# Performance work log

Hardware: AMD Instinct MI355X
Metric: run time of the kernel (lower is better)

Reference implementation:

```python
import jax, jax.numpy as jnp
import numpy as np

N_NODES = 100000
N_EDGES = 1280000
D_IN = 64
D_HID = 64


def _sage_conv(x, src, dst, deg, Wl, bl, Wr):
    # gather source-node features per edge, scatter-mean to destination nodes
    msg = x[src]                                            # [E, d]
    agg = jax.ops.segment_sum(msg, dst, num_segments=N_NODES)  # [N, d]
    mean = agg / deg                                        # [N, d]
    # PyG SAGEConv: lin_l(aggregated) + lin_r(root); bias lives in lin_l
    return mean @ Wl.T + bl + x @ Wr.T


def setup_inputs() -> dict:
    key = jax.random.key(0)
    ks = jax.random.split(key, 10)
    x = jax.random.normal(ks[0], (N_NODES, D_IN), dtype=jnp.float32)
    edge_index = jax.random.randint(ks[1], (2, N_EDGES), 0, N_NODES, dtype=jnp.int64)
    s = 1.0 / np.sqrt(D_IN)
    W1l = jax.random.uniform(ks[2], (D_HID, D_IN), jnp.float32, -s, s)
    W1r = jax.random.uniform(ks[3], (D_HID, D_IN), jnp.float32, -s, s)
    b1 = jax.random.uniform(ks[4], (D_HID,), jnp.float32, -s, s)
    s2 = 1.0 / np.sqrt(D_HID)
    W2l = jax.random.uniform(ks[5], (D_HID, D_HID), jnp.float32, -s2, s2)
    W2r = jax.random.uniform(ks[6], (D_HID, D_HID), jnp.float32, -s2, s2)
    b2 = jax.random.uniform(ks[7], (D_HID,), jnp.float32, -s2, s2)
    Wh = jax.random.uniform(ks[8], (1, D_HID), jnp.float32, -s2, s2)
    bh = jax.random.uniform(ks[9], (1,), jnp.float32, -s2, s2)
    return {"x": x, "edge_index": edge_index, "W1l": W1l, "W1r": W1r, "b1": b1,
            "W2l": W2l, "W2r": W2r, "b2": b2, "Wh": Wh, "bh": bh}


def reference(x, edge_index, W1l, W1r, b1, W2l, W2r, b2, Wh, bh):
    src, dst = edge_index[0], edge_index[1]
    # in-degree for mean aggregation (clamped to avoid div-by-zero)
    deg = jax.ops.segment_sum(jnp.ones((N_EDGES,), jnp.float32), dst,
                              num_segments=N_NODES)
    deg = jnp.maximum(deg, 1.0)[:, None]                    # [N, 1]
    h = jax.nn.relu(_sage_conv(x, src, dst, deg, W1l, b1, W1r))
    h = jax.nn.relu(_sage_conv(h, src, dst, deg, W2l, b2, W2r))
    out = (h @ Wh.T + bh)[:, 0]                             # [N]
    return out, h
```

## Files before the change

kernel.cpp:

```cpp
#include <hip/hip_runtime.h>

#define N_NODES 100000
#define N_EDGES 1280000
#define D 64
#define NPAD 102400
#define CAP 48
#define NBUCK 391
#define AB 313
#define CVB 1024
#define NT32 3125
#define XQ (N_NODES * 16)

typedef __attribute__((ext_vector_type(8))) short bf16x8;
typedef __attribute__((ext_vector_type(4))) float f32x4;
typedef __attribute__((ext_vector_type(2))) float f32x2;

__device__ __forceinline__ unsigned short f2bf(float f) {
    union { float f; unsigned u; } c; c.f = f;
    unsigned u = c.u;
    return (unsigned short)((u + 0x7FFF + ((u >> 16) & 1)) >> 16);
}
__device__ __forceinline__ float bf2f(unsigned short s) {
    union { unsigned u; float f; } c; c.u = ((unsigned)s) << 16;
    return c.f;
}
__device__ __forceinline__ float fp8d(unsigned b) {
    unsigned t = ((b & 0x80u) << 24) | ((b & 0x7fu) << 20);
    union { unsigned u; float f; } c; c.u = t;
    return c.f * 1.32922799578491587e36f;
}
__device__ __forceinline__ unsigned char f2fp8(float f) {
    f = fminf(fmaxf(f, -448.f), 448.f);
    float g = f * 7.52316384526264005e-37f;
    union { float f; unsigned u; } c; c.f = g;
    unsigned gb = c.u;
    unsigned r = (((gb & 0x7fffffffu) + 0x7ffffu + ((gb >> 20) & 1u)) >> 20) & 0x7fu;
    return (unsigned char)(((gb >> 24) & 0x80u) | r);
}

__global__ __launch_bounds__(512) void prep_kernel(
    const float* __restrict__ x,
    const int* __restrict__ src, const int* __restrict__ dst,
    const float* __restrict__ W1l, const float* __restrict__ W1r,
    const float* __restrict__ W2l, const float* __restrict__ W2r,
    unsigned short* __restrict__ xb, unsigned short* __restrict__ h1b,
    unsigned char* __restrict__ x8, unsigned char* __restrict__ h8,
    unsigned short* __restrict__ wb,
    int* __restrict__ sorted, int* __restrict__ exclT)
{
    __shared__ int cntA[392];
    __shared__ int excl[512];
    __shared__ int stage_pk[4096];

    const int t   = threadIdx.x;
    const int bid = blockIdx.x;

    if (bid < AB) {
        const int e0 = bid * 4096;
        const int cbatch = min(4096, N_EDGES - e0);

        if (t < 392) cntA[t] = 0;
        __syncthreads();

        int mb[8], mr[8], mpk[8];
#pragma unroll
        for (int i = 0; i < 8; ++i) {
            int idx = i * 512 + t;
            mb[i] = -1;
            if (idx < cbatch) {
                int e = e0 + idx;
                int s = src[e], d = dst[e];
                int b = d >> 8;
                mb[i]  = b;
                mpk[i] = (s << 8) | (d & 255);
                mr[i]  = atomicAdd(&cntA[b], 1);
            }
        }
        __syncthreads();

        excl[t] = (t < 392) ? cntA[t] : 0;
        __syncthreads();
        for (int off = 1; off < 512; off <<= 1) {
            int u = (t >= off) ? excl[t - off] : 0;
            __syncthreads();
            excl[t] += u;
            __syncthreads();
        }

#pragma unroll
        for (int i = 0; i < 8; ++i) {
            if (mb[i] >= 0) {
                int b = mb[i];
                stage_pk[excl[b] - cntA[b] + mr[i]] = mpk[i];
            }
        }
        __syncthreads();

#pragma unroll
        for (int i = 0; i < 8; ++i) {
            int idx = i * 512 + t;
            if (idx < cbatch) sorted[e0 + idx] = stage_pk[idx];
        }
        if (t < 392) exclT[bid * 392 + t] = excl[t] - cntA[t];
    } else {
        const int gtid = (bid - AB) * 512 + t;
        const int gsz  = CVB * 512;
        const int TOT  = XQ + 32 + 4096;
        for (int i = gtid; i < TOT; i += gsz) {
            if (i < XQ) {
                float4 v = ((const float4*)x)[i];
                ((ushort4*)xb)[i] = make_ushort4(f2bf(v.x), f2bf(v.y), f2bf(v.z), f2bf(v.w));
                ((uchar4*)x8)[i]  = make_uchar4(f2fp8(v.x), f2fp8(v.y), f2fp8(v.z), f2fp8(v.w));
            } else if (i < XQ + 32) {
                int k = i - XQ;
                if (k < 16) {
                    ((ushort4*)xb)[(size_t)N_NODES * 16 + k] = make_ushort4(0,0,0,0);
                    ((unsigned*)x8)[(size_t)N_NODES * 16 + k] = 0u;
                } else {
                    ((ushort4*)h1b)[(size_t)N_NODES * 16 + (k - 16)] = make_ushort4(0,0,0,0);
                    ((unsigned*)h8)[(size_t)N_NODES * 16 + (k - 16)] = 0u;
                }
            } else {
                int wf = i - XQ - 32;
                int m = wf >> 10, k = wf & 1023;
                const float* s = (m == 0) ? W1l : (m == 1) ? W1r : (m == 2) ? W2l : W2r;
                float4 v = ((const float4*)s)[k];
                ((ushort4*)wb)[m * 1024 + k] =
                    make_ushort4(f2bf(v.x), f2bf(v.y), f2bf(v.z), f2bf(v.w));
            }
        }
    }
}

__global__ __launch_bounds__(512) void binB_kernel(const int* __restrict__ sorted,
                                                   const int* __restrict__ exclT,
                                                   int* __restrict__ csr,
                                                   int* __restrict__ deg) {
    __shared__ int cur[256];
    __shared__ __align__(16) int lcsr[256 * CAP];
    __shared__ int scan[512];
    __shared__ int segstart[314];
    __shared__ int segsrc[313];

    const int t = threadIdx.x;
    const int k = blockIdx.x;

    if (t < 256) cur[t] = 0;

    int cnt = 0, s0 = 0;
    if (t < AB) {
        s0  = exclT[t * 392 + k];
        cnt = exclT[t * 392 + k + 1] - s0;
    }
    scan[t] = (t < AB) ? cnt : 0;
    __syncthreads();
    for (int off = 1; off < 512; off <<= 1) {
        int u = (t >= off) ? scan[t - off] : 0;
        __syncthreads();
        scan[t] += u;
        __syncthreads();
    }
    if (t < AB) {
        segstart[t] = scan[t] - cnt;
        segsrc[t]   = t * 4096 + s0;
    }
    if (t == AB - 1) segstart[AB] = scan[AB - 1];
    __syncthreads();

    const int Tk = segstart[AB];
    for (int i = t; i < Tk; i += 512) {
        int lo = 0, hi = AB;
        while (hi - lo > 1) {
            int mid = (lo + hi) >> 1;
            if (segstart[mid] <= i) lo = mid; else hi = mid;
        }
        int pk = sorted[segsrc[lo] + (i - segstart[lo])];
        int nl = pk & 255;
        int s  = pk >> 8;
        int r  = atomicAdd(&cur[nl], 1);
        if (r < CAP) lcsr[nl * CAP + r] = s;
    }
    __syncthreads();

    const int base = k * 256;
    for (int i = t; i < 4096; i += 512) {
        int r = i >> 4, c = i & 15;
        if (c < 12) {
            int lenr = min(cur[r], CAP);
            if (c * 4 < lenr)
                *(int4*)(csr + (size_t)(base + r) * CAP + c * 4) =
                    *(const int4*)(lcsr + r * CAP + c * 4);
        }
    }
    if (t < 256) deg[base + t] = cur[t];
}

template <int LAYER>
__global__ __launch_bounds__(512) void layer_kernel(
    const int* __restrict__ csr, const int* __restrict__ deg_g,
    const unsigned char*  __restrict__ feat8,
    const unsigned short* __restrict__ root_b,
    const unsigned short* __restrict__ wl_b,
    const float* __restrict__ bl,
    const unsigned short* __restrict__ wr_b,
    unsigned short* __restrict__ hout_b,
    unsigned char*  __restrict__ hout8,
    float* __restrict__ hout_f,
    const float* __restrict__ Wh, const float* __restrict__ bh,
    float* __restrict__ out)
{
    __shared__ __align__(16) char lds[10240];
    unsigned short* sA = (unsigned short*)lds;
    unsigned short* sX = sA + 32 * 72;
    float* sH    = (float*)lds;
    float* spart = (float*)(lds + 9216);

    const int tid = threadIdx.x;
    const int n0  = blockIdx.x * 32;

    {
        int row = tid >> 4, c4 = tid & 15;
        ushort4 x4 = ((const ushort4*)root_b)[(n0 + row) * 16 + c4];
        *(ushort4*)(sX + row * 72 + c4 * 4) = x4;
    }

    {
        const uint2* fb2 = (const uint2*)feat8;
        const int g   = tid >> 4;
        const int l   = tid & 15;
        const int h   = l >> 3;
        const int lo  = l & 7;
        const int n   = n0 + g;
        const int dg  = deg_g[n];
        const int len = (dg < CAP) ? dg : CAP;
        const int* rp = csr + n * CAP;
        f32x2 a0 = {0.f, 0.f}, a1 = {0.f, 0.f}, a2 = {0.f, 0.f}, a3 = {0.f, 0.f};
        for (int cb = 0; cb < len; cb += 16) {
            int idxl = cb + l;
            int id = (idxl < len) ? rp[idxl] : N_NODES;
            uint2 w[8];
#pragma unroll
            for (int i = 0; i < 8; ++i)
                w[i] = fb2[(__shfl(id, 2 * i + h, 16) << 3) + lo];
#pragma unroll
            for (int i = 0; i < 8; ++i) {
#if __has_builtin(__builtin_amdgcn_cvt_pk_f32_fp8)
                a0 += __builtin_amdgcn_cvt_pk_f32_fp8((int)w[i].x, false);
                a1 += __builtin_amdgcn_cvt_pk_f32_fp8((int)w[i].x, true);
                a2 += __builtin_amdgcn_cvt_pk_f32_fp8((int)w[i].y, false);
                a3 += __builtin_amdgcn_cvt_pk_f32_fp8((int)w[i].y, true);
#else
                f32x2 p0 = {fp8d(w[i].x & 255), fp8d((w[i].x >> 8) & 255)};
                f32x2 p1 = {fp8d((w[i].x >> 16) & 255), fp8d(w[i].x >> 24)};
                f32x2 p2 = {fp8d(w[i].y & 255), fp8d((w[i].y >> 8) & 255)};
                f32x2 p3 = {fp8d((w[i].y >> 16) & 255), fp8d(w[i].y >> 24)};
                a0 += p0; a1 += p1; a2 += p2; a3 += p3;
#endif
            }
        }
        a0.x += __shfl_xor(a0.x, 8); a0.y += __shfl_xor(a0.y, 8);
        a1.x += __shfl_xor(a1.x, 8); a1.y += __shfl_xor(a1.y, 8);
        a2.x += __shfl_xor(a2.x, 8); a2.y += __shfl_xor(a2.y, 8);
        a3.x += __shfl_xor(a3.x, 8); a3.y += __shfl_xor(a3.y, 8);
        float inv = 1.0f / fmaxf((float)dg, 1.0f);
        if (h == 0) {
            *(ushort4*)(sA + g * 72 + lo * 8) =
                make_ushort4(f2bf(a0.x * inv), f2bf(a0.y * inv),
                             f2bf(a1.x * inv), f2bf(a1.y * inv));
            *(ushort4*)(sA + g * 72 + lo * 8 + 4) =
                make_ushort4(f2bf(a2.x * inv), f2bf(a2.y * inv),
                             f2bf(a3.x * inv), f2bf(a3.y * inv));
        }
    }
    __syncthreads();

    const int w8 = tid >> 6;
    const int rt = w8 & 1, jt = w8 >> 1;
    const int l64 = tid & 63;
    const int rowl = l64 & 15, quad = l64 >> 4;

    const unsigned short* ap = sA + (rt * 16 + rowl) * 72 + quad * 8;
    const unsigned short* xp = sX + (rt * 16 + rowl) * 72 + quad * 8;
    bf16x8 am0 = *(const bf16x8*)(ap);
    bf16x8 am1 = *(const bf16x8*)(ap + 32);
    bf16x8 ax0 = *(const bf16x8*)(xp);
    bf16x8 ax1 = *(const bf16x8*)(xp + 32);
    __syncthreads();

    const unsigned short* wlp = wl_b + (jt * 16 + rowl) * 64 + quad * 8;
    const unsigned short* wrp = wr_b + (jt * 16 + rowl) * 64 + quad * 8;
    bf16x8 b0 = *(const bf16x8*)(wlp);
    bf16x8 b1 = *(const bf16x8*)(wlp + 32);
    bf16x8 b2 = *(const bf16x8*)(wrp);
    bf16x8 b3 = *(const bf16x8*)(wrp + 32);
    f32x4 acc = {0.f, 0.f, 0.f, 0.f};
    acc = __builtin_amdgcn_mfma_f32_16x16x32_bf16(am0, b0, acc, 0, 0, 0);
    acc = __builtin_amdgcn_mfma_f32_16x16x32_bf16(am1, b1, acc, 0, 0, 0);
    acc = __builtin_amdgcn_mfma_f32_16x16x32_bf16(ax0, b2, acc, 0, 0, 0);
    acc = __builtin_amdgcn_mfma_f32_16x16x32_bf16(ax1, b3, acc, 0, 0, 0);
    float bj = bl[jt * 16 + rowl];

#pragma unroll
    for (int r = 0; r < 4; ++r) {
        int node = rt * 16 + quad * 4 + r;
        sH[node * 68 + jt * 16 + rowl] = fmaxf(acc[r] + bj, 0.f);
    }
    __syncthreads();

    if (LAYER == 2 && tid < 256) {
        int node = tid >> 3, q = tid & 7;
        float p = 0.f;
#pragma unroll
        for (int c = 0; c < 2; ++c) {
            float4 hv = *(const float4*)(sH + node * 68 + q * 8 + c * 4);
            float4 wv = ((const float4*)Wh)[q * 2 + c];
            p += hv.x * wv.x + hv.y * wv.y + hv.z * wv.z + hv.w * wv.w;
        }
        spart[tid] = p;
    }

    {
        int row = tid >> 4, c4 = tid & 15;
        int n = n0 + row;
        const float* hp = sH + row * 68 + c4 * 4;
        if (LAYER == 1) {
            ((ushort4*)hout_b)[n * 16 + c4] =
                make_ushort4(f2bf(hp[0]), f2bf(hp[1]), f2bf(hp[2]), f2bf(hp[3]));
            ((uchar4*)hout8)[n * 16 + c4] =
                make_uchar4(f2fp8(hp[0]), f2fp8(hp[1]), f2fp8(hp[2]), f2fp8(hp[3]));
        } else {
            ((float4*)hout_f)[n * 16 + c4] =
                make_float4(hp[0], hp[1], hp[2], hp[3]);
        }
    }

    if (LAYER == 2) {
        __syncthreads();
        if (tid < 32) {
            float s = bh[0];
#pragma unroll
            for (int q = 0; q < 8; ++q) s += spart[tid * 8 + q];
            out[n0 + tid] = s;
        }
    }
}

extern "C" void kernel_launch(void* const* d_in, const int* in_sizes, int n_in,
                              void* d_out, int out_size, void* d_ws, size_t ws_size,
                              hipStream_t stream) {
    const float* x   = (const float*)d_in[0];
    const int*   ei  = (const int*)d_in[1];
    const int*   src = ei;
    const int*   dst = ei + N_EDGES;
    const float* W1l = (const float*)d_in[2];
    const float* W1r = (const float*)d_in[3];
    const float* b1  = (const float*)d_in[4];
    const float* W2l = (const float*)d_in[5];
    const float* W2r = (const float*)d_in[6];
    const float* b2  = (const float*)d_in[7];
    const float* Wh  = (const float*)d_in[8];
    const float* bh  = (const float*)d_in[9];

    float* out   = (float*)d_out;
    float* h_out = out + N_NODES;

    int* wsi = (int*)d_ws;
    int* deg = wsi;
    int* csr = deg + NPAD;
    unsigned short* wb  = (unsigned short*)(csr + NBUCK * 256 * CAP);
    unsigned short* x_b = wb + 16384;
    unsigned short* h1b = x_b + (size_t)(N_NODES + 1) * D;
    unsigned char*  x8  = (unsigned char*)(h1b + (size_t)(N_NODES + 1) * D);
    unsigned char*  h8  = x8 + (size_t)(N_NODES + 1) * D;
    int* sorted = (int*)h1b;
    int* exclT  = sorted + AB * 4096;

    unsigned short* w1l_b = wb;
    unsigned short* w1r_b = wb + 4096;
    unsigned short* w2l_b = wb + 8192;
    unsigned short* w2r_b = wb + 12288;

    prep_kernel<<<AB + CVB, 512, 0, stream>>>(
        x, src, dst, W1l, W1r, W2l, W2r, x_b, h1b, x8, h8, wb, sorted, exclT);

    binB_kernel<<<NBUCK, 512, 0, stream>>>(sorted, exclT, csr, deg);

    layer_kernel<1><<<NT32, 512, 0, stream>>>(
        csr, deg, x8, x_b, w1l_b, b1, w1r_b, h1b, h8, nullptr,
        nullptr, nullptr, nullptr);
    layer_kernel<2><<<NT32, 512, 0, stream>>>(
        csr, deg, h8, h1b, w2l_b, b2, w2r_b, nullptr, nullptr, h_out,
        Wh, bh, out);
}
```

Measured before the change: 181.7 us.

## Fuse all four kernels into one persistent kernel with grid barriers

Replaces the prep, binning and two layer launches with a single persistent kernel that loops over the same work items and separates phases with atomic-counter grid barriers. The grid is sized from the occupancy query and capped at 512 blocks, and a memset resets the barrier counter before each launch. The aim is to remove launch gaps and tail effects between the four kernels. In exchange it adds barrier spin overhead and a larger shared-memory footprint, which may lower occupancy during the layer phases. It also relies on every block being co-resident.

```diff
diff --git a/kernel.cpp b/kernel.cpp
--- a/kernel.cpp
+++ b/kernel.cpp
@@ -7,9 +7,13 @@
 #define CAP 48
 #define NBUCK 391
 #define AB 313
-#define CVB 1024
+#define NCVT 711
 #define NT32 3125
 #define XQ (N_NODES * 16)
+#define CVTOT (XQ + 32 + 4096)
+#define CVW ((CVTOT + NCVT - 1) / NCVT)
+#define GRID 512
+#define SMEM_BYTES 52688
 
 typedef __attribute__((ext_vector_type(8))) short bf16x8;
 typedef __attribute__((ext_vector_type(4))) float f32x4;
@@ -19,10 +23,6 @@
     union { float f; unsigned u; } c; c.f = f;
     unsigned u = c.u;
     return (unsigned short)((u + 0x7FFF + ((u >> 16) & 1)) >> 16);
-}
-__device__ __forceinline__ float bf2f(unsigned short s) {
-    union { unsigned u; float f; } c; c.u = ((unsigned)s) << 16;
-    return c.f;
 }
 __device__ __forceinline__ float fp8d(unsigned b) {
     unsigned t = ((b & 0x80u) << 24) | ((b & 0x7fu) << 20);
@@ -38,185 +38,32 @@
     return (unsigned char)(((gb >> 24) & 0x80u) | r);
 }
 
-__global__ __launch_bounds__(512) void prep_kernel(
-    const float* __restrict__ x,
-    const int* __restrict__ src, const int* __restrict__ dst,
-    const float* __restrict__ W1l, const float* __restrict__ W1r,
-    const float* __restrict__ W2l, const float* __restrict__ W2r,
-    unsigned short* __restrict__ xb, unsigned short* __restrict__ h1b,
-    unsigned char* __restrict__ x8, unsigned char* __restrict__ h8,
-    unsigned short* __restrict__ wb,
-    int* __restrict__ sorted, int* __restrict__ exclT)
+__device__ __forceinline__ void grid_sync(int* bar, int target) {
+    __syncthreads();
+    if (threadIdx.x == 0) {
+        __threadfence();
+        atomicAdd(bar, 1);
+        while (__hip_atomic_load(bar, __ATOMIC_RELAXED,
+                                 __HIP_MEMORY_SCOPE_AGENT) < target)
+            __builtin_amdgcn_s_sleep(2);
+        __threadfence();
+    }
+    __syncthreads();
+}
+
+template <int LAYER>
+__device__ void layer_phase(int n0, char* lds,
+    const int* csr, const int* deg_g,
+    const unsigned char* feat8, const unsigned short* root_b,
+    const unsigned short* wl_b, const float* bl, const unsigned short* wr_b,
+    unsigned short* hout_b, unsigned char* hout8, float* hout_f,
+    const float* Wh, const float* bh, float* out)
 {
-    __shared__ int cntA[392];
-    __shared__ int excl[512];
-    __shared__ int stage_pk[4096];
-
-    const int t   = threadIdx.x;
-    const int bid = blockIdx.x;
-
-    if (bid < AB) {
-        const int e0 = bid * 4096;
-        const int cbatch = min(4096, N_EDGES - e0);
-
-        if (t < 392) cntA[t] = 0;
-        __syncthreads();
-
-        int mb[8], mr[8], mpk[8];
-#pragma unroll
-        for (int i = 0; i < 8; ++i) {
-            int idx = i * 512 + t;
-            mb[i] = -1;
-            if (idx < cbatch) {
-                int e = e0 + idx;
-                int s = src[e], d = dst[e];
-                int b = d >> 8;
-                mb[i]  = b;
-                mpk[i] = (s << 8) | (d & 255);
-                mr[i]  = atomicAdd(&cntA[b], 1);
-            }
-        }
-        __syncthreads();
-
-        excl[t] = (t < 392) ? cntA[t] : 0;
-        __syncthreads();
-        for (int off = 1; off < 512; off <<= 1) {
-            int u = (t >= off) ? excl[t - off] : 0;
-            __syncthreads();
-            excl[t] += u;
-            __syncthreads();
-        }
-
-#pragma unroll
-        for (int i = 0; i < 8; ++i) {
-            if (mb[i] >= 0) {
-                int b = mb[i];
-                stage_pk[excl[b] - cntA[b] + mr[i]] = mpk[i];
-            }
-        }
-        __syncthreads();
-
-#pragma unroll
-        for (int i = 0; i < 8; ++i) {
-            int idx = i * 512 + t;
-            if (idx < cbatch) sorted[e0 + idx] = stage_pk[idx];
-        }
-        if (t < 392) exclT[bid * 392 + t] = excl[t] - cntA[t];
-    } else {
-        const int gtid = (bid - AB) * 512 + t;
-        const int gsz  = CVB * 512;
-        const int TOT  = XQ + 32 + 4096;
-        for (int i = gtid; i < TOT; i += gsz) {
-            if (i < XQ) {
-                float4 v = ((const float4*)x)[i];
-                ((ushort4*)xb)[i] = make_ushort4(f2bf(v.x), f2bf(v.y), f2bf(v.z), f2bf(v.w));
-                ((uchar4*)x8)[i]  = make_uchar4(f2fp8(v.x), f2fp8(v.y), f2fp8(v.z), f2fp8(v.w));
-            } else if (i < XQ + 32) {
-                int k = i - XQ;
-                if (k < 16) {
-                    ((ushort4*)xb)[(size_t)N_NODES * 16 + k] = make_ushort4(0,0,0,0);
-                    ((unsigned*)x8)[(size_t)N_NODES * 16 + k] = 0u;
-                } else {
-                    ((ushort4*)h1b)[(size_t)N_NODES * 16 + (k - 16)] = make_ushort4(0,0,0,0);
-                    ((unsigned*)h8)[(size_t)N_NODES * 16 + (k - 16)] = 0u;
-                }
-            } else {
-                int wf = i - XQ - 32;
-                int m = wf >> 10, k = wf & 1023;
-                const float* s = (m == 0) ? W1l : (m == 1) ? W1r : (m == 2) ? W2l : W2r;
-                float4 v = ((const float4*)s)[k];
-                ((ushort4*)wb)[m * 1024 + k] =
-                    make_ushort4(f2bf(v.x), f2bf(v.y), f2bf(v.z), f2bf(v.w));
-            }
-        }
-    }
-}
-
-__global__ __launch_bounds__(512) void binB_kernel(const int* __restrict__ sorted,
-                                                   const int* __restrict__ exclT,
-                                                   int* __restrict__ csr,
-                                                   int* __restrict__ deg) {
-    __shared__ int cur[256];
-    __shared__ __align__(16) int lcsr[256 * CAP];
-    __shared__ int scan[512];
-    __shared__ int segstart[314];
-    __shared__ int segsrc[313];
-
-    const int t = threadIdx.x;
-    const int k = blockIdx.x;
-
-    if (t < 256) cur[t] = 0;
-
-    int cnt = 0, s0 = 0;
-    if (t < AB) {
-        s0  = exclT[t * 392 + k];
-        cnt = exclT[t * 392 + k + 1] - s0;
-    }
-    scan[t] = (t < AB) ? cnt : 0;
-    __syncthreads();
-    for (int off = 1; off < 512; off <<= 1) {
-        int u = (t >= off) ? scan[t - off] : 0;
-        __syncthreads();
-        scan[t] += u;
-        __syncthreads();
-    }
-    if (t < AB) {
-        segstart[t] = scan[t] - cnt;
-        segsrc[t]   = t * 4096 + s0;
-    }
-    if (t == AB - 1) segstart[AB] = scan[AB - 1];
-    __syncthreads();
-
-    const int Tk = segstart[AB];
-    for (int i = t; i < Tk; i += 512) {
-        int lo = 0, hi = AB;
-        while (hi - lo > 1) {
-            int mid = (lo + hi) >> 1;
-            if (segstart[mid] <= i) lo = mid; else hi = mid;
-        }
-        int pk = sorted[segsrc[lo] + (i - segstart[lo])];
-        int nl = pk & 255;
-        int s  = pk >> 8;
-        int r  = atomicAdd(&cur[nl], 1);
-        if (r < CAP) lcsr[nl * CAP + r] = s;
-    }
-    __syncthreads();
-
-    const int base = k * 256;
-    for (int i = t; i < 4096; i += 512) {
-        int r = i >> 4, c = i & 15;
-        if (c < 12) {
-            int lenr = min(cur[r], CAP);
-            if (c * 4 < lenr)
-                *(int4*)(csr + (size_t)(base + r) * CAP + c * 4) =
-                    *(const int4*)(lcsr + r * CAP + c * 4);
-        }
-    }
-    if (t < 256) deg[base + t] = cur[t];
-}
-
-template <int LAYER>
-__global__ __launch_bounds__(512) void layer_kernel(
-    const int* __restrict__ csr, const int* __restrict__ deg_g,
-    const unsigned char*  __restrict__ feat8,
-    const unsigned short* __restrict__ root_b,
-    const unsigned short* __restrict__ wl_b,
-    const float* __restrict__ bl,
-    const unsigned short* __restrict__ wr_b,
-    unsigned short* __restrict__ hout_b,
-    unsigned char*  __restrict__ hout8,
-    float* __restrict__ hout_f,
-    const float* __restrict__ Wh, const float* __restrict__ bh,
-    float* __restrict__ out)
-{
-    __shared__ __align__(16) char lds[10240];
     unsigned short* sA = (unsigned short*)lds;
     unsigned short* sX = sA + 32 * 72;
     float* sH    = (float*)lds;
     float* spart = (float*)(lds + 9216);
-
     const int tid = threadIdx.x;
-    const int n0  = blockIdx.x * 32;
 
     {
         int row = tid >> 4, c4 = tid & 15;
@@ -343,6 +190,180 @@
             out[n0 + tid] = s;
         }
     }
+    __syncthreads();
+}
+
+__global__ __launch_bounds__(512, 4) void fused_kernel(
+    const float* __restrict__ x,
+    const int* __restrict__ srcp, const int* __restrict__ dstp,
+    const float* __restrict__ W1l, const float* __restrict__ W1r,
+    const float* __restrict__ b1v,
+    const float* __restrict__ W2l, const float* __restrict__ W2r,
+    const float* __restrict__ b2v,
+    const float* __restrict__ Whp, const float* __restrict__ bhp,
+    unsigned short* __restrict__ xb, unsigned short* h1b,
+    unsigned char* __restrict__ x8, unsigned char* __restrict__ h8,
+    unsigned short* __restrict__ wb,
+    int* sorted, int* exclT,
+    int* __restrict__ csr, int* __restrict__ deg,
+    float* __restrict__ h_out, float* __restrict__ outp,
+    int* bar)
+{
+    __shared__ __align__(16) char smem[SMEM_BYTES];
+    const int tid = threadIdx.x;
+    const int bid = blockIdx.x;
+    const int nb  = gridDim.x;
+
+    for (int w = bid; w < AB + NCVT; w += nb) {
+        if (w < AB) {
+            int* cntA     = (int*)smem;
+            int* excl     = cntA + 392;
+            int* stage_pk = excl + 512;
+            const int e0 = w * 4096;
+            const int cbatch = min(4096, N_EDGES - e0);
+            __syncthreads();
+            if (tid < 392) cntA[tid] = 0;
+            __syncthreads();
+
+            int mb[8], mr[8], mpk[8];
+#pragma unroll
+            for (int i = 0; i < 8; ++i) {
+                int idx = i * 512 + tid;
+                mb[i] = -1;
+                if (idx < cbatch) {
+                    int e = e0 + idx;
+                    int s = srcp[e], d = dstp[e];
+                    int b = d >> 8;
+                    mb[i]  = b;
+                    mpk[i] = (s << 8) | (d & 255);
+                    mr[i]  = atomicAdd(&cntA[b], 1);
+                }
+            }
+            __syncthreads();
+
+            excl[tid] = (tid < 392) ? cntA[tid] : 0;
+            __syncthreads();
+            for (int off = 1; off < 512; off <<= 1) {
+                int u = (tid >= off) ? excl[tid - off] : 0;
+                __syncthreads();
+                excl[tid] += u;
+                __syncthreads();
+            }
+
+#pragma unroll
+            for (int i = 0; i < 8; ++i) {
+                if (mb[i] >= 0) {
+                    int b = mb[i];
+                    stage_pk[excl[b] - cntA[b] + mr[i]] = mpk[i];
+                }
+            }
+            __syncthreads();
+
+#pragma unroll
+            for (int i = 0; i < 8; ++i) {
+                int idx = i * 512 + tid;
+                if (idx < cbatch) sorted[e0 + idx] = stage_pk[idx];
+            }
+            if (tid < 392) exclT[w * 392 + tid] = excl[tid] - cntA[tid];
+        } else {
+            const int c  = w - AB;
+            const int lo = c * CVW;
+            const int hi = min(CVTOT, lo + CVW);
+            for (int i = lo + tid; i < hi; i += 512) {
+                if (i < XQ) {
+                    float4 v = ((const float4*)x)[i];
+                    ((ushort4*)xb)[i] = make_ushort4(f2bf(v.x), f2bf(v.y), f2bf(v.z), f2bf(v.w));
+                    ((uchar4*)x8)[i]  = make_uchar4(f2fp8(v.x), f2fp8(v.y), f2fp8(v.z), f2fp8(v.w));
+                } else if (i < XQ + 32) {
+                    int kk = i - XQ;
+                    if (kk < 16) {
+                        ((ushort4*)xb)[(size_t)N_NODES * 16 + kk] = make_ushort4(0,0,0,0);
+                        ((unsigned*)x8)[(size_t)N_NODES * 16 + kk] = 0u;
+                    } else {
+                        ((ushort4*)h1b)[(size_t)N_NODES * 16 + (kk - 16)] = make_ushort4(0,0,0,0);
+                        ((unsigned*)h8)[(size_t)N_NODES * 16 + (kk - 16)] = 0u;
+                    }
+                } else {
+                    int wf = i - XQ - 32;
+                    int m = wf >> 10, kk = wf & 1023;
+                    const float* s = (m == 0) ? W1l : (m == 1) ? W1r : (m == 2) ? W2l : W2r;
+                    float4 v = ((const float4*)s)[kk];
+                    ((ushort4*)wb)[m * 1024 + kk] =
+                        make_ushort4(f2bf(v.x), f2bf(v.y), f2bf(v.z), f2bf(v.w));
+                }
+            }
+        }
+    }
+    grid_sync(bar, nb);
+
+    for (int k = bid; k < NBUCK; k += nb) {
+        int* lcsr     = (int*)smem;
+        int* scan     = (int*)smem;
+        int* cur      = lcsr + 256 * CAP;
+        int* segstart = cur + 256;
+        int* segsrc   = segstart + 314;
+        __syncthreads();
+        if (tid < 256) cur[tid] = 0;
+
+        int cnt = 0, s0 = 0;
+        if (tid < AB) {
+            s0  = exclT[tid * 392 + k];
+            cnt = exclT[tid * 392 + k + 1] - s0;
+        }
+        scan[tid] = (tid < AB) ? cnt : 0;
+        __syncthreads();
+        for (int off = 1; off < 512; off <<= 1) {
+            int u = (tid >= off) ? scan[tid - off] : 0;
+            __syncthreads();
+            scan[tid] += u;
+            __syncthreads();
+        }
+        if (tid < AB) {
+            segstart[tid] = scan[tid] - cnt;
+            segsrc[tid]   = tid * 4096 + s0;
+        }
+        if (tid == AB - 1) segstart[AB] = scan[AB - 1];
+        __syncthreads();
+
+        const int Tk = segstart[AB];
+        for (int i = tid; i < Tk; i += 512) {
+            int lo2 = 0, hi2 = AB;
+            while (hi2 - lo2 > 1) {
+                int mid = (lo2 + hi2) >> 1;
+                if (segstart[mid] <= i) lo2 = mid; else hi2 = mid;
+            }
+            int pk = sorted[segsrc[lo2] + (i - segstart[lo2])];
+            int nl = pk & 255;
+            int s  = pk >> 8;
+            int r  = atomicAdd(&cur[nl], 1);
+            if (r < CAP) lcsr[nl * CAP + r] = s;
+        }
+        __syncthreads();
+
+        const int base = k * 256;
+        for (int i = tid; i < 4096; i += 512) {
+            int r = i >> 4, cc = i & 15;
+            if (cc < 12) {
+                int lenr = min(cur[r], CAP);
+                if (cc * 4 < lenr)
+                    *(int4*)(csr + (size_t)(base + r) * CAP + cc * 4) =
+                        *(const int4*)(lcsr + r * CAP + cc * 4);
+            }
+        }
+        if (tid < 256) deg[base + tid] = cur[tid];
+    }
+    grid_sync(bar, 2 * nb);
+
+    for (int tdx = bid; tdx < NT32; tdx += nb)
+        layer_phase<1>(tdx * 32, smem, csr, deg, x8, xb,
+                       wb, b1v, wb + 4096, h1b, h8, nullptr,
+                       nullptr, nullptr, nullptr);
+    grid_sync(bar, 3 * nb);
+
+    for (int tdx = bid; tdx < NT32; tdx += nb)
+        layer_phase<2>(tdx * 32, smem, csr, deg, h8, h1b,
+                       wb + 8192, b2v, wb + 12288, nullptr, nullptr, h_out,
+                       Whp, bhp, outp);
 }
 
 extern "C" void kernel_launch(void* const* d_in, const int* in_sizes, int n_in,
@@ -365,7 +386,8 @@
     float* h_out = out + N_NODES;
 
     int* wsi = (int*)d_ws;
-    int* deg = wsi;
+    int* bar = wsi;
+    int* deg = wsi + 64;
     int* csr = deg + NPAD;
     unsigned short* wb  = (unsigned short*)(csr + NBUCK * 256 * CAP);
     unsigned short* x_b = wb + 16384;
@@ -375,20 +397,18 @@
     int* sorted = (int*)h1b;
     int* exclT  = sorted + AB * 4096;
 
-    unsigned short* w1l_b = wb;
-    unsigned short* w1r_b = wb + 4096;
-    unsigned short* w2l_b = wb + 8192;
-    unsigned short* w2r_b = wb + 12288;
-
-    prep_kernel<<<AB + CVB, 512, 0, stream>>>(
-        x, src, dst, W1l, W1r, W2l, W2r, x_b, h1b, x8, h8, wb, sorted, exclT);
-
-    binB_kernel<<<NBUCK, 512, 0, stream>>>(sorted, exclT, csr, deg);
-
-    layer_kernel<1><<<NT32, 512, 0, stream>>>(
-        csr, deg, x8, x_b, w1l_b, b1, w1r_b, h1b, h8, nullptr,
-        nullptr, nullptr, nullptr);
-    layer_kernel<2><<<NT32, 512, 0, stream>>>(
-        csr, deg, h8, h1b, w2l_b, b2, w2r_b, nullptr, nullptr, h_out,
-        Wh, bh, out);
-}
+    static int nblk = 0;
+    if (nblk == 0) {
+        int nb2 = 0;
+        if (hipOccupancyMaxActiveBlocksPerMultiprocessor(&nb2, fused_kernel, 512, 0)
+                != hipSuccess || nb2 < 1)
+            nb2 = 1;
+        nblk = nb2 * 256;
+        if (nblk > GRID) nblk = GRID;
+    }
+
+    hipMemsetAsync(bar, 0, 256, stream);
+    fused_kernel<<<nblk, 512, 0, stream>>>(
+        x, src, dst, W1l, W1r, b1, W2l, W2r, b2, Wh, bh,
+        x_b, h1b, x8, h8, wb, sorted, exclT, csr, deg, h_out, out, bar);
+}
```

After: 309.1 us. 1.7x slower.

## Build CSR directly with global atomics instead of two-pass bucket sort

Applied to the files above, without the earlier changes.

Replaces the two-kernel local bucket sort (per-block LDS histogram plus scan, then per-bucket gather into LDS CSR) with a single kernel in which each edge does a global atomicAdd on its destination degree and writes its source straight into a fixed-capacity CSR row. A memset clears the degree array, and feature conversion runs in the same kernel after the edge loop. This removes a kernel launch and the intermediate sorted buffer, but it adds 1.28M contended global atomics and scattered 4-byte writes. Neighbor order within a row now depends on atomic timing, which can change the floating-point summation order.

```diff
diff --git a/kernel.cpp b/kernel.cpp
--- a/kernel.cpp
+++ b/kernel.cpp
@@ -5,11 +5,10 @@
 #define D 64
 #define NPAD 102400
 #define CAP 48
-#define NBUCK 391
-#define AB 313
-#define CVB 1024
 #define NT32 3125
 #define XQ (N_NODES * 16)
+#define CVTOT (XQ + 32 + 4096)
+#define PB 2048
 
 typedef __attribute__((ext_vector_type(8))) short bf16x8;
 typedef __attribute__((ext_vector_type(4))) float f32x4;
@@ -19,10 +18,6 @@
     union { float f; unsigned u; } c; c.f = f;
     unsigned u = c.u;
     return (unsigned short)((u + 0x7FFF + ((u >> 16) & 1)) >> 16);
-}
-__device__ __forceinline__ float bf2f(unsigned short s) {
-    union { unsigned u; float f; } c; c.u = ((unsigned)s) << 16;
-    return c.f;
 }
 __device__ __forceinline__ float fp8d(unsigned b) {
     unsigned t = ((b & 0x80u) << 24) | ((b & 0x7fu) << 20);
@@ -38,7 +33,7 @@
     return (unsigned char)(((gb >> 24) & 0x80u) | r);
 }
 
-__global__ __launch_bounds__(512) void prep_kernel(
+__global__ __launch_bounds__(256) void prep2_kernel(
     const float* __restrict__ x,
     const int* __restrict__ src, const int* __restrict__ dst,
     const float* __restrict__ W1l, const float* __restrict__ W1r,
@@ -46,153 +41,40 @@
     unsigned short* __restrict__ xb, unsigned short* __restrict__ h1b,
     unsigned char* __restrict__ x8, unsigned char* __restrict__ h8,
     unsigned short* __restrict__ wb,
-    int* __restrict__ sorted, int* __restrict__ exclT)
+    int* __restrict__ csr, int* __restrict__ deg)
 {
-    __shared__ int cntA[392];
-    __shared__ int excl[512];
-    __shared__ int stage_pk[4096];
-
-    const int t   = threadIdx.x;
-    const int bid = blockIdx.x;
-
-    if (bid < AB) {
-        const int e0 = bid * 4096;
-        const int cbatch = min(4096, N_EDGES - e0);
-
-        if (t < 392) cntA[t] = 0;
-        __syncthreads();
-
-        int mb[8], mr[8], mpk[8];
-#pragma unroll
-        for (int i = 0; i < 8; ++i) {
-            int idx = i * 512 + t;
-            mb[i] = -1;
-            if (idx < cbatch) {
-                int e = e0 + idx;
-                int s = src[e], d = dst[e];
-                int b = d >> 8;
-                mb[i]  = b;
-                mpk[i] = (s << 8) | (d & 255);
-                mr[i]  = atomicAdd(&cntA[b], 1);
+    const int gt = blockIdx.x * 256 + threadIdx.x;
+    const int gs = PB * 256;
+
+    for (int e = gt; e < N_EDGES; e += gs) {
+        int s = src[e], d = dst[e];
+        int r = atomicAdd(&deg[d], 1);
+        if (r < CAP) csr[(size_t)d * CAP + r] = s;
+    }
+
+    for (int i = gt; i < CVTOT; i += gs) {
+        if (i < XQ) {
+            float4 v = ((const float4*)x)[i];
+            ((ushort4*)xb)[i] = make_ushort4(f2bf(v.x), f2bf(v.y), f2bf(v.z), f2bf(v.w));
+            ((uchar4*)x8)[i]  = make_uchar4(f2fp8(v.x), f2fp8(v.y), f2fp8(v.z), f2fp8(v.w));
+        } else if (i < XQ + 32) {
+            int k = i - XQ;
+            if (k < 16) {
+                ((ushort4*)xb)[(size_t)N_NODES * 16 + k] = make_ushort4(0,0,0,0);
+                ((unsigned*)x8)[(size_t)N_NODES * 16 + k] = 0u;
+            } else {
+                ((ushort4*)h1b)[(size_t)N_NODES * 16 + (k - 16)] = make_ushort4(0,0,0,0);
+                ((unsigned*)h8)[(size_t)N_NODES * 16 + (k - 16)] = 0u;
             }
-        }
-        __syncthreads();
-
-        excl[t] = (t < 392) ? cntA[t] : 0;
-        __syncthreads();
-        for (int off = 1; off < 512; off <<= 1) {
-            int u = (t >= off) ? excl[t - off] : 0;
-            __syncthreads();
-            excl[t] += u;
-            __syncthreads();
-        }
-
-#pragma unroll
-        for (int i = 0; i < 8; ++i) {
-            if (mb[i] >= 0) {
-                int b = mb[i];
-                stage_pk[excl[b] - cntA[b] + mr[i]] = mpk[i];
-            }
-        }
-        __syncthreads();
-
-#pragma unroll
-        for (int i = 0; i < 8; ++i) {
-            int idx = i * 512 + t;
-            if (idx < cbatch) sorted[e0 + idx] = stage_pk[idx];
-        }
-        if (t < 392) exclT[bid * 392 + t] = excl[t] - cntA[t];
-    } else {
-        const int gtid = (bid - AB) * 512 + t;
-        const int gsz  = CVB * 512;
-        const int TOT  = XQ + 32 + 4096;
-        for (int i = gtid; i < TOT; i += gsz) {
-            if (i < XQ) {
-                float4 v = ((const float4*)x)[i];
-                ((ushort4*)xb)[i] = make_ushort4(f2bf(v.x), f2bf(v.y), f2bf(v.z), f2bf(v.w));
-                ((uchar4*)x8)[i]  = make_uchar4(f2fp8(v.x), f2fp8(v.y), f2fp8(v.z), f2fp8(v.w));
-            } else if (i < XQ + 32) {
-                int k = i - XQ;
-                if (k < 16) {
-                    ((ushort4*)xb)[(size_t)N_NODES * 16 + k] = make_ushort4(0,0,0,0);
-                    ((unsigned*)x8)[(size_t)N_NODES * 16 + k] = 0u;
-                } else {
-                    ((ushort4*)h1b)[(size_t)N_NODES * 16 + (k - 16)] = make_ushort4(0,0,0,0);
-                    ((unsigned*)h8)[(size_t)N_NODES * 16 + (k - 16)] = 0u;
-                }
-            } else {
-                int wf = i - XQ - 32;
-                int m = wf >> 10, k = wf & 1023;
-                const float* s = (m == 0) ? W1l : (m == 1) ? W1r : (m == 2) ? W2l : W2r;
-                float4 v = ((const float4*)s)[k];
-                ((ushort4*)wb)[m * 1024 + k] =
-                    make_ushort4(f2bf(v.x), f2bf(v.y), f2bf(v.z), f2bf(v.w));
-            }
-        }
-    }
-}
-
-__global__ __launch_bounds__(512) void binB_kernel(const int* __restrict__ sorted,
-                                                   const int* __restrict__ exclT,
-                                                   int* __restrict__ csr,
-                                                   int* __restrict__ deg) {
-    __shared__ int cur[256];
-    __shared__ __align__(16) int lcsr[256 * CAP];
-    __shared__ int scan[512];
-    __shared__ int segstart[314];
-    __shared__ int segsrc[313];
-
-    const int t = threadIdx.x;
-    const int k = blockIdx.x;
-
-    if (t < 256) cur[t] = 0;
-
-    int cnt = 0, s0 = 0;
-    if (t < AB) {
-        s0  = exclT[t * 392 + k];
-        cnt = exclT[t * 392 + k + 1] - s0;
-    }
-    scan[t] = (t < AB) ? cnt : 0;
-    __syncthreads();
-    for (int off = 1; off < 512; off <<= 1) {
-        int u = (t >= off) ? scan[t - off] : 0;
-        __syncthreads();
-        scan[t] += u;
-        __syncthreads();
-    }
-    if (t < AB) {
-        segstart[t] = scan[t] - cnt;
-        segsrc[t]   = t * 4096 + s0;
-    }
-    if (t == AB - 1) segstart[AB] = scan[AB - 1];
-    __syncthreads();
-
-    const int Tk = segstart[AB];
-    for (int i = t; i < Tk; i += 512) {
-        int lo = 0, hi = AB;
-        while (hi - lo > 1) {
-            int mid = (lo + hi) >> 1;
-            if (segstart[mid] <= i) lo = mid; else hi = mid;
-        }
-        int pk = sorted[segsrc[lo] + (i - segstart[lo])];
-        int nl = pk & 255;
-        int s  = pk >> 8;
-        int r  = atomicAdd(&cur[nl], 1);
-        if (r < CAP) lcsr[nl * CAP + r] = s;
-    }
-    __syncthreads();
-
-    const int base = k * 256;
-    for (int i = t; i < 4096; i += 512) {
-        int r = i >> 4, c = i & 15;
-        if (c < 12) {
-            int lenr = min(cur[r], CAP);
-            if (c * 4 < lenr)
-                *(int4*)(csr + (size_t)(base + r) * CAP + c * 4) =
-                    *(const int4*)(lcsr + r * CAP + c * 4);
-        }
-    }
-    if (t < 256) deg[base + t] = cur[t];
+        } else {
+            int wf = i - XQ - 32;
+            int m = wf >> 10, k = wf & 1023;
+            const float* s = (m == 0) ? W1l : (m == 1) ? W1r : (m == 2) ? W2l : W2r;
+            float4 v = ((const float4*)s)[k];
+            ((ushort4*)wb)[m * 1024 + k] =
+                make_ushort4(f2bf(v.x), f2bf(v.y), f2bf(v.z), f2bf(v.w));
+        }
+    }
 }
 
 template <int LAYER>
@@ -233,7 +115,7 @@
         const int n   = n0 + g;
         const int dg  = deg_g[n];
         const int len = (dg < CAP) ? dg : CAP;
-        const int* rp = csr + n * CAP;
+        const int* rp = csr + (size_t)n * CAP;
         f32x2 a0 = {0.f, 0.f}, a1 = {0.f, 0.f}, a2 = {0.f, 0.f}, a3 = {0.f, 0.f};
         for (int cb = 0; cb < len; cb += 16) {
             int idxl = cb + l;
@@ -367,23 +249,21 @@
     int* wsi = (int*)d_ws;
     int* deg = wsi;
     int* csr = deg + NPAD;
-    unsigned short* wb  = (unsigned short*)(csr + NBUCK * 256 * CAP);
+    unsigned short* wb  = (unsigned short*)(csr + (size_t)NPAD * CAP);
     unsigned short* x_b = wb + 16384;
     unsigned short* h1b = x_b + (size_t)(N_NODES + 1) * D;
     unsigned char*  x8  = (unsigned char*)(h1b + (size_t)(N_NODES + 1) * D);
     unsigned char*  h8  = x8 + (size_t)(N_NODES + 1) * D;
-    int* sorted = (int*)h1b;
-    int* exclT  = sorted + AB * 4096;
 
     unsigned short* w1l_b = wb;
     unsigned short* w1r_b = wb + 4096;
     unsigned short* w2l_b = wb + 8192;
     unsigned short* w2r_b = wb + 12288;
 
-    prep_kernel<<<AB + CVB, 512, 0, stream>>>(
-        x, src, dst, W1l, W1r, W2l, W2r, x_b, h1b, x8, h8, wb, sorted, exclT);
-
-    binB_kernel<<<NBUCK, 512, 0, stream>>>(sorted, exclT, csr, deg);
+    hipMemsetAsync(deg, 0, NPAD * sizeof(int), stream);
+
+    prep2_kernel<<<PB, 256, 0, stream>>>(
+        x, src, dst, W1l, W1r, W2l, W2r, x_b, h1b, x8, h8, wb, csr, deg);
 
     layer_kernel<1><<<NT32, 512, 0, stream>>>(
         csr, deg, x8, x_b, w1l_b, b1, w1r_b, h1b, h8, nullptr,
```

Result: slower. 264.0 us (+45.3%).

## Replace LDS scans with wave scans, serial per-segment binning, and prefetch first CSR chunk

Applied to the files above, without the earlier changes.

Prep's 512-wide block scan with many barriers becomes a single-wave shuffle scan over 7-element per-thread partials, storing exclusive offsets directly. binB drops its block scan and binary search; each thread now walks one source batch's segment serially with a one-ahead prefetch. The layer kernel loads the first 16 CSR indices before the degree-dependent loop, so the first gather chunk no longer waits on the degree load. The serial walk in binB may load-imbalance threads and lose memory coalescing compared with the old flat-index distribution.

```diff
diff --git a/kernel.cpp b/kernel.cpp
--- a/kernel.cpp
+++ b/kernel.cpp
@@ -19,10 +19,6 @@
     union { float f; unsigned u; } c; c.f = f;
     unsigned u = c.u;
     return (unsigned short)((u + 0x7FFF + ((u >> 16) & 1)) >> 16);
-}
-__device__ __forceinline__ float bf2f(unsigned short s) {
-    union { unsigned u; float f; } c; c.u = ((unsigned)s) << 16;
-    return c.f;
 }
 __device__ __forceinline__ float fp8d(unsigned b) {
     unsigned t = ((b & 0x80u) << 24) | ((b & 0x7fu) << 20);
@@ -49,7 +45,7 @@
     int* __restrict__ sorted, int* __restrict__ exclT)
 {
     __shared__ int cntA[392];
-    __shared__ int excl[512];
+    __shared__ int excl[392];
     __shared__ int stage_pk[4096];
 
     const int t   = threadIdx.x;
@@ -78,21 +74,30 @@
         }
         __syncthreads();
 
-        excl[t] = (t < 392) ? cntA[t] : 0;
+        if (t < 64) {
+            int pre[7], tot = 0;
+            if (t < 56) {
+#pragma unroll
+                for (int i = 0; i < 7; ++i) { pre[i] = tot; tot += cntA[t * 7 + i]; }
+            }
+            int sc = tot;
+#pragma unroll
+            for (int off = 1; off < 64; off <<= 1) {
+                int u = __shfl_up(sc, off, 64);
+                if (t >= off) sc += u;
+            }
+            int ex = sc - tot;
+            if (t < 56) {
+#pragma unroll
+                for (int i = 0; i < 7; ++i) excl[t * 7 + i] = ex + pre[i];
+            }
+        }
         __syncthreads();
-        for (int off = 1; off < 512; off <<= 1) {
-            int u = (t >= off) ? excl[t - off] : 0;
-            __syncthreads();
-            excl[t] += u;
-            __syncthreads();
-        }
 
 #pragma unroll
         for (int i = 0; i < 8; ++i) {
-            if (mb[i] >= 0) {
-                int b = mb[i];
-                stage_pk[excl[b] - cntA[b] + mr[i]] = mpk[i];
-            }
+            if (mb[i] >= 0)
+                stage_pk[excl[mb[i]] + mr[i]] = mpk[i];
         }
         __syncthreads();
 
@@ -101,7 +106,7 @@
             int idx = i * 512 + t;
             if (idx < cbatch) sorted[e0 + idx] = stage_pk[idx];
         }
-        if (t < 392) exclT[bid * 392 + t] = excl[t] - cntA[t];
+        if (t < 392) exclT[bid * 392 + t] = excl[t];
     } else {
         const int gtid = (bid - AB) * 512 + t;
         const int gsz  = CVB * 512;
@@ -138,58 +143,38 @@
                                                    int* __restrict__ deg) {
     __shared__ int cur[256];
     __shared__ __align__(16) int lcsr[256 * CAP];
-    __shared__ int scan[512];
-    __shared__ int segstart[314];
-    __shared__ int segsrc[313];
 
     const int t = threadIdx.x;
     const int k = blockIdx.x;
 
     if (t < 256) cur[t] = 0;
-
-    int cnt = 0, s0 = 0;
+    __syncthreads();
+
     if (t < AB) {
-        s0  = exclT[t * 392 + k];
-        cnt = exclT[t * 392 + k + 1] - s0;
-    }
-    scan[t] = (t < AB) ? cnt : 0;
-    __syncthreads();
-    for (int off = 1; off < 512; off <<= 1) {
-        int u = (t >= off) ? scan[t - off] : 0;
-        __syncthreads();
-        scan[t] += u;
-        __syncthreads();
-    }
-    if (t < AB) {
-        segstart[t] = scan[t] - cnt;
-        segsrc[t]   = t * 4096 + s0;
-    }
-    if (t == AB - 1) segstart[AB] = scan[AB - 1];
-    __syncthreads();
-
-    const int Tk = segstart[AB];
-    for (int i = t; i < Tk; i += 512) {
-        int lo = 0, hi = AB;
-        while (hi - lo > 1) {
-            int mid = (lo + hi) >> 1;
-            if (segstart[mid] <= i) lo = mid; else hi = mid;
-        }
-        int pk = sorted[segsrc[lo] + (i - segstart[lo])];
-        int nl = pk & 255;
-        int s  = pk >> 8;
-        int r  = atomicAdd(&cur[nl], 1);
-        if (r < CAP) lcsr[nl * CAP + r] = s;
+        int s0  = exclT[t * 392 + k];
+        int cnt = exclT[t * 392 + k + 1] - s0;
+        const int* sp = sorted + t * 4096 + s0;
+        if (cnt > 0) {
+            int pk = sp[0];
+            for (int e = 0; e < cnt; ++e) {
+                int nxt = (e + 1 < cnt) ? sp[e + 1] : 0;
+                int nl = pk & 255;
+                int r  = atomicAdd(&cur[nl], 1);
+                if (r < CAP) lcsr[nl * CAP + r] = pk >> 8;
+                pk = nxt;
+            }
+        }
     }
     __syncthreads();
 
     const int base = k * 256;
     for (int i = t; i < 4096; i += 512) {
-        int r = i >> 4, c = i & 15;
-        if (c < 12) {
+        int r = i >> 4, cc = i & 15;
+        if (cc < 12) {
             int lenr = min(cur[r], CAP);
-            if (c * 4 < lenr)
-                *(int4*)(csr + (size_t)(base + r) * CAP + c * 4) =
-                    *(const int4*)(lcsr + r * CAP + c * 4);
+            if (cc * 4 < lenr)
+                *(int4*)(csr + (size_t)(base + r) * CAP + cc * 4) =
+                    *(const int4*)(lcsr + r * CAP + cc * 4);
         }
     }
     if (t < 256) deg[base + t] = cur[t];
@@ -231,33 +216,54 @@
         const int h   = l >> 3;
         const int lo  = l & 7;
         const int n   = n0 + g;
+        const int* rp = csr + (size_t)n * CAP;
         const int dg  = deg_g[n];
+        const int id0 = rp[l];
         const int len = (dg < CAP) ? dg : CAP;
-        const int* rp = csr + n * CAP;
         f32x2 a0 = {0.f, 0.f}, a1 = {0.f, 0.f}, a2 = {0.f, 0.f}, a3 = {0.f, 0.f};
-        for (int cb = 0; cb < len; cb += 16) {
+
+#if __has_builtin(__builtin_amdgcn_cvt_pk_f32_fp8)
+#define GCHUNK(IDEXPR)                                                       \
+        {                                                                    \
+            int id_ = (IDEXPR);                                              \
+            uint2 w[8];                                                      \
+            _Pragma("unroll")                                                \
+            for (int i = 0; i < 8; ++i)                                      \
+                w[i] = fb2[(__shfl(id_, 2 * i + h, 16) << 3) + lo];          \
+            _Pragma("unroll")                                                \
+            for (int i = 0; i < 8; ++i) {                                    \
+                a0 += __builtin_amdgcn_cvt_pk_f32_fp8((int)w[i].x, false);   \
+                a1 += __builtin_amdgcn_cvt_pk_f32_fp8((int)w[i].x, true);    \
+                a2 += __builtin_amdgcn_cvt_pk_f32_fp8((int)w[i].y, false);   \
+                a3 += __builtin_amdgcn_cvt_pk_f32_fp8((int)w[i].y, true);    \
+            }                                                                \
+        }
+#else
+#define GCHUNK(IDEXPR)                                                       \
+        {                                                                    \
+            int id_ = (IDEXPR);                                              \
+            uint2 w[8];                                                      \
+            _Pragma("unroll")                                                \
+            for (int i = 0; i < 8; ++i)                                      \
+                w[i] = fb2[(__shfl(id_, 2 * i + h, 16) << 3) + lo];          \
+            _Pragma("unroll")                                                \
+            for (int i = 0; i < 8; ++i) {                                    \
+                f32x2 p0 = {fp8d(w[i].x & 255), fp8d((w[i].x >> 8) & 255)};  \
+                f32x2 p1 = {fp8d((w[i].x >> 16) & 255), fp8d(w[i].x >> 24)}; \
+                f32x2 p2 = {fp8d(w[i].y & 255), fp8d((w[i].y >> 8) & 255)};  \
+                f32x2 p3 = {fp8d((w[i].y >> 16) & 255), fp8d(w[i].y >> 24)}; \
+                a0 += p0; a1 += p1; a2 += p2; a3 += p3;                      \
+            }                                                                \
+        }
+#endif
+
+        GCHUNK((l < len) ? id0 : N_NODES);
+        for (int cb = 16; cb < len; cb += 16) {
             int idxl = cb + l;
-            int id = (idxl < len) ? rp[idxl] : N_NODES;
-            uint2 w[8];
-#pragma unroll
-            for (int i = 0; i < 8; ++i)
-                w[i] = fb2[(__shfl(id, 2 * i + h, 16) << 3) + lo];
-#pragma unroll
-            for (int i = 0; i < 8; ++i) {
-#if __has_builtin(__builtin_amdgcn_cvt_pk_f32_fp8)
-                a0 += __builtin_amdgcn_cvt_pk_f32_fp8((int)w[i].x, false);
-                a1 += __builtin_amdgcn_cvt_pk_f32_fp8((int)w[i].x, true);
-                a2 += __builtin_amdgcn_cvt_pk_f32_fp8((int)w[i].y, false);
-                a3 += __builtin_amdgcn_cvt_pk_f32_fp8((int)w[i].y, true);
-#else
-                f32x2 p0 = {fp8d(w[i].x & 255), fp8d((w[i].x >> 8) & 255)};
-                f32x2 p1 = {fp8d((w[i].x >> 16) & 255), fp8d(w[i].x >> 24)};
-                f32x2 p2 = {fp8d(w[i].y & 255), fp8d((w[i].y >> 8) & 255)};
-                f32x2 p3 = {fp8d((w[i].y >> 16) & 255), fp8d(w[i].y >> 24)};
-                a0 += p0; a1 += p1; a2 += p2; a3 += p3;
-#endif
-            }
-        }
+            GCHUNK((idxl < len) ? rp[idxl] : N_NODES);
+        }
+#undef GCHUNK
+
         a0.x += __shfl_xor(a0.x, 8); a0.y += __shfl_xor(a0.y, 8);
         a1.x += __shfl_xor(a1.x, 8); a1.y += __shfl_xor(a1.y, 8);
         a2.x += __shfl_xor(a2.x, 8); a2.y += __shfl_xor(a2.y, 8);
```

Result: no change. 178.9 us (-1.5%).
